# Optimization experiments

Hardware: AMD Instinct MI355X
Metric: run time of the kernel (lower is better)

## Reference

```python
import jax, jax.numpy as jnp
import numpy as np

N_NODES = 50000
N_EDGES = 800000


def _inv_sqrt_deg(idx, n):
    deg = jax.ops.segment_sum(jnp.ones(idx.shape, jnp.float32), idx, num_segments=n)
    return jnp.where(deg > 0, deg ** -0.5, 0.0)


def graph_conv(x, W, b, src, dst, norm_src, norm_dst):
    # DGL GraphConv, norm='both': D_dst^{-1/2} A D_src^{-1/2} X W + b
    # Apply weight before aggregation (out_feats < in_feats in both layers).
    h = (x * norm_src[:, None]) @ W            # [N, out]
    m = h[src]                                  # gather per-edge messages [E, out]
    agg = jax.ops.segment_sum(m, dst, num_segments=x.shape[0])
    return agg * norm_dst[:, None] + b


def setup_inputs() -> dict:
    key = jax.random.key(0)
    ks = jax.random.split(key, 6)
    x = jax.random.normal(ks[0], (N_NODES, 512), jnp.float32)
    W1 = jax.random.normal(ks[1], (512, 128), jnp.float32) * (512 ** -0.5)
    b1 = jnp.zeros((128,), jnp.float32)
    W2 = jax.random.normal(ks[2], (128, 40), jnp.float32) * (128 ** -0.5)
    b2 = jnp.zeros((40,), jnp.float32)
    src = jax.random.randint(ks[3], (N_EDGES,), 0, N_NODES, jnp.int32)
    dst = jax.random.randint(ks[4], (N_EDGES,), 0, N_NODES, jnp.int32)
    return {"x": x, "W1": W1, "b1": b1, "W2": W2, "b2": b2, "src": src, "dst": dst}


def reference(x, W1, b1, W2, b2, src, dst):
    n = x.shape[0]
    norm_src = _inv_sqrt_deg(src, n)  # out-degree based src norm
    norm_dst = _inv_sqrt_deg(dst, n)  # in-degree based dst norm
    h = graph_conv(x, W1, b1, src, dst, norm_src, norm_dst)
    h = jax.nn.relu(h)
    h = graph_conv(h, W2, b2, src, dst, norm_src, norm_dst)
    return h
```

## Files before the change

### kernel.cpp

```cpp
#include <hip/hip_runtime.h>
#include <hip/hip_bf16.h>

#define F0 512
#define F1 128
#define F2 40

#define NRP 12800
#define G_SL 64

typedef __attribute__((ext_vector_type(8))) short bf16x8;
typedef __attribute__((ext_vector_type(4))) float f32x4;

__device__ inline ushort f2bf(float f) {
    union { float f; uint u; } v; v.f = f;
    uint u = v.u;
    uint r = u + 0x7fffu + ((u >> 16) & 1u);
    return (ushort)(r >> 16);
}

#define CVT2(dst, a, b) { __hip_bfloat162 _t2 = __float22bfloat162_rn(make_float2(a, b)); __builtin_memcpy(&dst, &_t2, 4); }

__global__ __launch_bounds__(1024)
void hist_kernel(const int* __restrict__ src, const int* __restrict__ dst,
                 uchar* __restrict__ Gsrc, uchar* __restrict__ Gdst,
                 const float* __restrict__ W1, ushort* __restrict__ Wt, int n, int E) {
    if (blockIdx.x < (F0 * F1) / 1024) {
        int idx = blockIdx.x * 1024 + threadIdx.x;
        int k = idx >> 7, nn = idx & 127;
        Wt[nn * F0 + k] = f2bf(W1[idx]);
    }
    __shared__ uint cs[NRP / 2];
    __shared__ uint cd[NRP / 2];
    const int p = blockIdx.x / G_SL;
    const int g = blockIdx.x % G_SL;
    const int base = p * NRP;
    for (int i = threadIdx.x; i < NRP / 2; i += 1024) { cs[i] = 0; cd[i] = 0; }
    __syncthreads();
    const int Epg = (E + G_SL - 1) / G_SL;
    const int e0 = g * Epg;
    const int e1 = min(E, e0 + Epg);
    for (int i = e0 + (int)threadIdx.x; i < e1; i += 1024) {
        int s = src[i], d = dst[i];
        unsigned so = (unsigned)(s - base);
        unsigned dd = (unsigned)(d - base);
        if (so < (unsigned)NRP) atomicAdd(&cs[so >> 1], 1u << ((so & 1) * 16));
        if (dd < (unsigned)NRP) atomicAdd(&cd[dd >> 1], 1u << ((dd & 1) * 16));
    }
    __syncthreads();
    const int lim = min(NRP, n - base);
    for (int i = threadIdx.x; i < lim; i += 1024) {
        uint pcs = cs[i >> 1], pcd = cd[i >> 1];
        int sh = (i & 1) * 16;
        Gsrc[(size_t)g * n + base + i] = (uchar)((pcs >> sh) & 0xffu);
        Gdst[(size_t)g * n + base + i] = (uchar)((pcd >> sh) & 0xffu);
    }
}

__global__ __launch_bounds__(256)
void scanA_kernel(const uchar* __restrict__ Gsrc, const uchar* __restrict__ Gdst,
                  float* __restrict__ norm_src, float* __restrict__ norm_dst,
                  int* __restrict__ row_off, int* __restrict__ bsum, int n) {
    __shared__ int sm[256];
    int i = blockIdx.x * 256 + threadIdx.x;
    int s = 0, d = 0;
    if (i < n) {
#pragma unroll
        for (int g = 0; g < G_SL; g++) {
            s += Gsrc[(size_t)g * n + i];
            d += Gdst[(size_t)g * n + i];
        }
        norm_src[i] = s > 0 ? rsqrtf((float)s) : 0.f;
        norm_dst[i] = d > 0 ? rsqrtf((float)d) : 0.f;
    }
    sm[threadIdx.x] = (i < n) ? d : 0;
    __syncthreads();
    for (int off = 1; off < 256; off <<= 1) {
        int t = (threadIdx.x >= (unsigned)off) ? sm[threadIdx.x - off] : 0;
        __syncthreads();
        sm[threadIdx.x] += t;
        __syncthreads();
    }
    if (i < n) row_off[i + 1] = sm[threadIdx.x];
    if (threadIdx.x == 255) bsum[blockIdx.x] = sm[255];
}

__global__ __launch_bounds__(256)
void finalize_kernel(int* __restrict__ row_off, const int* __restrict__ bsum,
                     const uchar* __restrict__ Gdst, int* __restrict__ Goff, int n) {
    __shared__ int sm[256];
    const int b = blockIdx.x;
    const int t = threadIdx.x;
    sm[t] = (t < b) ? bsum[t] : 0;
    __syncthreads();
#pragma unroll
    for (int off = 128; off > 0; off >>= 1) {
        if (t < off) sm[t] += sm[t + off];
        __syncthreads();
    }
    const int excl = sm[0];
    const int v = b * 256 + t;
    if (v >= n) return;
    int raw = row_off[v];
    int start = excl + ((t == 0) ? 0 : raw);
    if (v == n - 1) {
        int rawn = row_off[n];
        row_off[n] = excl + rawn;
    }
    row_off[v] = start;
    int run = start;
#pragma unroll
    for (int g = 0; g < G_SL; g++) {
        size_t idx = (size_t)g * n + v;
        Goff[idx] = run;
        run += Gdst[idx];
    }
}

#define BM 64

union SmemU {
    int cur[NRP];
    char Al[2][8192];
};

#define ISSUE(kt, buf) {                                                               \
    __builtin_amdgcn_global_load_lds(                                                  \
        (const __attribute__((address_space(1))) void*)(gsrc_base + (kt) * 32),        \
        (__attribute__((address_space(3))) void*)(&smu.Al[buf][tid * 16]),             \
        16, 0, 0); }

#define LOADB(k0, b) { b = *reinterpret_cast<const bf16x8*>(bp + (k0)); }

#define MKFRAG(dst, mi, bufp) {                                                        \
    const int _row = (mi) * 16 + l15;                                                  \
    const char* _pr = (bufp) + _row * 128;                                             \
    float4 _pa = *reinterpret_cast<const float4*>(_pr + (((2 * lq + 0) ^ (_row & 7)) << 4)); \
    float4 _pb = *reinterpret_cast<const float4*>(_pr + (((2 * lq + 1) ^ (_row & 7)) << 4)); \
    union { uint u[4]; bf16x8 v; } _pk;                                                \
    CVT2(_pk.u[0], _pa.x, _pa.y); CVT2(_pk.u[1], _pa.z, _pa.w);                        \
    CVT2(_pk.u[2], _pb.x, _pb.y); CVT2(_pk.u[3], _pb.z, _pb.w);                        \
    dst = _pk.v; }

#define COMPUTE(buf, b) {                                                              \
    const char* _bp = &smu.Al[buf][0];                                                 \
    bf16x8 _a0, _a1, _a2, _a3;                                                         \
    MKFRAG(_a0, 0, _bp); MKFRAG(_a1, 1, _bp); MKFRAG(_a2, 2, _bp); MKFRAG(_a3, 3, _bp);\
    acc[0] = __builtin_amdgcn_mfma_f32_16x16x32_bf16(_a0, b, acc[0], 0, 0, 0);         \
    acc[1] = __builtin_amdgcn_mfma_f32_16x16x32_bf16(_a1, b, acc[1], 0, 0, 0);         \
    acc[2] = __builtin_amdgcn_mfma_f32_16x16x32_bf16(_a2, b, acc[2], 0, 0, 0);         \
    acc[3] = __builtin_amdgcn_mfma_f32_16x16x32_bf16(_a3, b, acc[3], 0, 0, 0); }

__global__ __launch_bounds__(512)
void place_gemm1_fused(const int* __restrict__ src, const int* __restrict__ dst,
                       const int* __restrict__ Goff, int* __restrict__ edge_src,
                       const float* __restrict__ x, const ushort* __restrict__ Wt,
                       const float* __restrict__ norm_src, ushort* __restrict__ h1g,
                       int n, int E, int ngemm) {
    __shared__ __align__(16) SmemU smu;
    const int tid = threadIdx.x;

    if (blockIdx.x >= ngemm) {
        const int pb = blockIdx.x - ngemm;
        const int p = pb / G_SL;
        const int g = pb % G_SL;
        const int base = p * NRP;
        const int lim = min(NRP, n - base);
        for (int i = tid; i < lim; i += 512)
            smu.cur[i] = Goff[(size_t)g * n + base + i];
        __syncthreads();
        const int Epg = (E + G_SL - 1) / G_SL;
        const int e0 = g * Epg;
        const int e1 = min(E, e0 + Epg);
        for (int i = e0 + tid; i < e1; i += 512) {
            int d = dst[i];
            unsigned dd = (unsigned)(d - base);
            if (dd < (unsigned)lim) {
                int pos = atomicAdd(&smu.cur[dd], 1);
                edge_src[pos] = src[i];
            }
        }
        return;
    }

    const int lane = tid & 63;
    const int w = tid >> 6;
    const int l15 = lane & 15;
    const int lq = lane >> 4;
    const int bm = blockIdx.x * BM;

    const int st_r = tid >> 3;
    const int st_c = (tid & 7) ^ (st_r & 7);
    int grow = bm + st_r;
    if (grow >= n) grow = n - 1;
    const float* gsrc_base = x + (size_t)grow * F0 + st_c * 4;

    const ushort* bp = Wt + (size_t)(w * 16 + l15) * F0 + lq * 8;

    f32x4 acc[4] = {};
    bf16x8 bcur, bnxt;

    ISSUE(0, 0);
    LOADB(0, bcur);
    __syncthreads();

    for (int kg = 0; kg < 16; ++kg) {
        const int cb = kg & 1;
        if (kg < 15) {
            ISSUE(kg + 1, cb ^ 1);
            LOADB((kg + 1) * 32, bnxt);
        }
        COMPUTE(cb, bcur);
        bcur = bnxt;
        if (kg < 15) __syncthreads();
    }

#pragma unroll
    for (int mi = 0; mi < 4; mi++) {
        int rbase = bm + mi * 16 + lq * 4;
#pragma unroll
        for (int r = 0; r < 4; r++) {
            int row = rbase + r;
            if (row < n) {
                float ns = norm_src[row];
                h1g[(size_t)row * F1 + w * 16 + l15] = f2bf(acc[mi][r] * ns);
            }
        }
    }
}

__global__ __launch_bounds__(256)
void agg1_kernel(const ushort* __restrict__ h1g, const int* __restrict__ row_off,
                 const int* __restrict__ edge_src, const float* __restrict__ norm_dst,
                 const float* __restrict__ b1, ushort* __restrict__ h1, int n) {
    int wid = (blockIdx.x * blockDim.x + threadIdx.x) >> 6;
    int lane = threadIdx.x & 63;
    if (wid >= n) return;
    int beg = row_off[wid], end = row_off[wid + 1];
    float a0 = 0.f, a1 = 0.f;
    int e = beg;
    for (; e + 7 < end; e += 8) {
        int s[8];
#pragma unroll
        for (int j = 0; j < 8; j++) s[j] = edge_src[e + j];
        uint v[8];
#pragma unroll
        for (int j = 0; j < 8; j++)
            v[j] = *reinterpret_cast<const uint*>(&h1g[(size_t)s[j] * F1 + lane * 2]);
#pragma unroll
        for (int j = 0; j < 8; j++) {
            a0 += __uint_as_float(v[j] << 16);
            a1 += __uint_as_float(v[j] & 0xffff0000u);
        }
    }
    for (; e < end; ++e) {
        int s = edge_src[e];
        uint v = *reinterpret_cast<const uint*>(&h1g[(size_t)s * F1 + lane * 2]);
        a0 += __uint_as_float(v << 16);
        a1 += __uint_as_float(v & 0xffff0000u);
    }
    float nd = norm_dst[wid];
    float o0 = fmaxf(a0 * nd + b1[lane * 2 + 0], 0.f);
    float o1 = fmaxf(a1 * nd + b1[lane * 2 + 1], 0.f);
    __hip_bfloat162 p2 = __float22bfloat162_rn(make_float2(o0, o1));
    uint pu; __builtin_memcpy(&pu, &p2, 4);
    *reinterpret_cast<uint*>(&h1[(size_t)wid * F1 + lane * 2]) = pu;
}

__global__ __launch_bounds__(256)
void gemm2_kernel(const ushort* __restrict__ h1, const float* __restrict__ W2,
                  const float* __restrict__ norm_src, ushort* __restrict__ h2g, int n) {
    __shared__ __align__(16) float W2s[F1][F2];
    for (int i = threadIdx.x; i < F1 * F2; i += 256)
        W2s[i / F2][i % F2] = W2[i];
    __syncthreads();
    int node = blockIdx.x * 256 + threadIdx.x;
    if (node >= n) return;
    float nrm = norm_src[node];
    f32x4 acc4[10] = {};
    const ushort* row = &h1[(size_t)node * F1];
    for (int kc = 0; kc < 16; kc++) {
        uint4 u = *reinterpret_cast<const uint4*>(&row[kc * 8]);
        uint uu[4] = {u.x, u.y, u.z, u.w};
        float f[8];
#pragma unroll
        for (int i = 0; i < 4; i++) {
            f[2 * i + 0] = __uint_as_float(uu[i] << 16);
            f[2 * i + 1] = __uint_as_float(uu[i] & 0xffff0000u);
        }
#pragma unroll
        for (int j = 0; j < 8; j++) {
#pragma unroll
            for (int c4 = 0; c4 < 10; c4++) {
                f32x4 wv = *reinterpret_cast<const f32x4*>(&W2s[kc * 8 + j][c4 * 4]);
                acc4[c4] += f[j] * wv;
            }
        }
    }
    ushort* orow = &h2g[(size_t)node * F2];
#pragma unroll
    for (int c4 = 0; c4 < 10; c4++) {
        f32x4 o = acc4[c4] * nrm;
        __hip_bfloat162 pa = __float22bfloat162_rn(make_float2(o[0], o[1]));
        __hip_bfloat162 pb = __float22bfloat162_rn(make_float2(o[2], o[3]));
        uint2 pk;
        __builtin_memcpy(&pk.x, &pa, 4);
        __builtin_memcpy(&pk.y, &pb, 4);
        *reinterpret_cast<uint2*>(&orow[c4 * 4]) = pk;
    }
}

__global__ __launch_bounds__(256)
void agg2_kernel(const ushort* __restrict__ h2g, const int* __restrict__ row_off,
                 const int* __restrict__ edge_src, const float* __restrict__ norm_dst,
                 const float* __restrict__ b2, float* __restrict__ out, int n) {
    int wid = (blockIdx.x * blockDim.x + threadIdx.x) >> 6;
    int lane = threadIdx.x & 63;
    if (wid >= n) return;
    int beg = row_off[wid], end = row_off[wid + 1];
    float a0 = 0.f, a1 = 0.f;
    int e = beg;
    const bool act = lane < 20;
    for (; e + 7 < end; e += 8) {
        int s[8];
#pragma unroll
        for (int j = 0; j < 8; j++) s[j] = edge_src[e + j];
        if (act) {
            uint v[8];
#pragma unroll
            for (int j = 0; j < 8; j++)
                v[j] = *reinterpret_cast<const uint*>(&h2g[(size_t)s[j] * F2 + lane * 2]);
#pragma unroll
            for (int j = 0; j < 8; j++) {
                a0 += __uint_as_float(v[j] << 16);
                a1 += __uint_as_float(v[j] & 0xffff0000u);
            }
        }
    }
    for (; e < end; ++e) {
        int s = edge_src[e];
        if (act) {
            uint v = *reinterpret_cast<const uint*>(&h2g[(size_t)s * F2 + lane * 2]);
            a0 += __uint_as_float(v << 16);
            a1 += __uint_as_float(v & 0xffff0000u);
        }
    }
    if (act) {
        float nd = norm_dst[wid];
        float o0 = a0 * nd + b2[lane * 2 + 0];
        float o1 = a1 * nd + b2[lane * 2 + 1];
        *reinterpret_cast<float2*>(&out[(size_t)wid * F2 + lane * 2]) = make_float2(o0, o1);
    }
}

extern "C" void kernel_launch(void* const* d_in, const int* in_sizes, int n_in,
                              void* d_out, int out_size, void* d_ws, size_t ws_size,
                              hipStream_t stream) {
    const float* x  = (const float*)d_in[0];
    const float* W1 = (const float*)d_in[1];
    const float* b1 = (const float*)d_in[2];
    const float* W2 = (const float*)d_in[3];
    const float* b2 = (const float*)d_in[4];
    const int* src  = (const int*)d_in[5];
    const int* dst  = (const int*)d_in[6];
    float* out = (float*)d_out;

    const int n = in_sizes[0] / F0;
    const int E = in_sizes[5];
    const int nb = (n + 255) / 256;
    const int P = (n + NRP - 1) / NRP;
    const int ngemm = (n + BM - 1) / BM;

    char* ws = (char*)d_ws;
    auto alloc = [&](size_t bytes) -> char* {
        char* p = ws;
        ws += (bytes + 255) & ~(size_t)255;
        return p;
    };
    int* row_off   = (int*)alloc((size_t)(n + 1) * 4);
    int* bsum      = (int*)alloc(256 * 4);
    int* edge_srcs = (int*)alloc((size_t)E * 4);
    float* norm_src_d = (float*)alloc((size_t)n * 4);
    float* norm_dst_d = (float*)alloc((size_t)n * 4);
    ushort* W1t = (ushort*)alloc((size_t)F1 * F0 * 2);
    ushort* h1g = (ushort*)alloc((size_t)n * F1 * 2);
    ushort* h1  = (ushort*)alloc((size_t)n * F1 * 2);
    ushort* h2g = h1g;

    uchar* Gsrc = (uchar*)h1g;
    uchar* Gdst = Gsrc + (size_t)G_SL * n;
    int* Goff = (int*)h1;

    hist_kernel<<<P * G_SL, 1024, 0, stream>>>(src, dst, Gsrc, Gdst, W1, W1t, n, E);
    scanA_kernel<<<nb, 256, 0, stream>>>(Gsrc, Gdst, norm_src_d, norm_dst_d, row_off, bsum, n);
    finalize_kernel<<<nb, 256, 0, stream>>>(row_off, bsum, Gdst, Goff, n);
    place_gemm1_fused<<<ngemm + P * G_SL, 512, 0, stream>>>(
        src, dst, Goff, edge_srcs, x, W1t, norm_src_d, h1g, n, E, ngemm);
    agg1_kernel<<<(n + 3) / 4, 256, 0, stream>>>(h1g, row_off, edge_srcs, norm_dst_d, b1, h1, n);
    gemm2_kernel<<<(n + 255) / 256, 256, 0, stream>>>(h1, W2, norm_src_d, h2g, n);
    agg2_kernel<<<(n + 3) / 4, 256, 0, stream>>>(h2g, row_off, edge_srcs, norm_dst_d, b2, out, n);
}
```

Before: 175.8 us.

## Deepen GEMM1 K-tile to 128 with four loads per stage, fewer barriers

Measured after the change: 181.7 us, median of 2. 3.3% more time.

```diff
diff --git a/kernel.cpp b/kernel.cpp
--- a/kernel.cpp
+++ b/kernel.cpp
@@ -117,38 +117,60 @@
 }
 
 #define BM 64
+#define NKT 4
 
 union SmemU {
     int cur[NRP];
-    char Al[2][8192];
+    char Al[2][32768];
 };
 
-#define ISSUE(kt, buf) {                                                               \
+#define ISSUE4(kt, buf) {                                                              \
     __builtin_amdgcn_global_load_lds(                                                  \
-        (const __attribute__((address_space(1))) void*)(gsrc_base + (kt) * 32),        \
+        (const __attribute__((address_space(1))) void*)(gs0 + (kt) * 128),             \
         (__attribute__((address_space(3))) void*)(&smu.Al[buf][tid * 16]),             \
+        16, 0, 0);                                                                     \
+    __builtin_amdgcn_global_load_lds(                                                  \
+        (const __attribute__((address_space(1))) void*)(gs1 + (kt) * 128),             \
+        (__attribute__((address_space(3))) void*)(&smu.Al[buf][8192 + tid * 16]),      \
+        16, 0, 0);                                                                     \
+    __builtin_amdgcn_global_load_lds(                                                  \
+        (const __attribute__((address_space(1))) void*)(gs2 + (kt) * 128),             \
+        (__attribute__((address_space(3))) void*)(&smu.Al[buf][16384 + tid * 16]),     \
+        16, 0, 0);                                                                     \
+    __builtin_amdgcn_global_load_lds(                                                  \
+        (const __attribute__((address_space(1))) void*)(gs3 + (kt) * 128),             \
+        (__attribute__((address_space(3))) void*)(&smu.Al[buf][24576 + tid * 16]),     \
         16, 0, 0); }
 
-#define LOADB(k0, b) { b = *reinterpret_cast<const bf16x8*>(bp + (k0)); }
-
-#define MKFRAG(dst, mi, bufp) {                                                        \
+#define LOADB4(kt, arr) {                                                              \
+    arr[0] = *reinterpret_cast<const bf16x8*>(bp + (kt) * 128 + 0);                    \
+    arr[1] = *reinterpret_cast<const bf16x8*>(bp + (kt) * 128 + 32);                   \
+    arr[2] = *reinterpret_cast<const bf16x8*>(bp + (kt) * 128 + 64);                   \
+    arr[3] = *reinterpret_cast<const bf16x8*>(bp + (kt) * 128 + 96); }
+
+#define MKFRAG(dst, mi, kk, bufp) {                                                    \
     const int _row = (mi) * 16 + l15;                                                  \
-    const char* _pr = (bufp) + _row * 128;                                             \
-    float4 _pa = *reinterpret_cast<const float4*>(_pr + (((2 * lq + 0) ^ (_row & 7)) << 4)); \
-    float4 _pb = *reinterpret_cast<const float4*>(_pr + (((2 * lq + 1) ^ (_row & 7)) << 4)); \
+    const char* _pr = (bufp) + _row * 512;                                             \
+    const int _sw = (l15 & 7) << 2;                                                    \
+    float4 _pa = *reinterpret_cast<const float4*>(_pr + ((((kk) * 8 + 2 * lq + 0) ^ _sw) << 4)); \
+    float4 _pb = *reinterpret_cast<const float4*>(_pr + ((((kk) * 8 + 2 * lq + 1) ^ _sw) << 4)); \
     union { uint u[4]; bf16x8 v; } _pk;                                                \
     CVT2(_pk.u[0], _pa.x, _pa.y); CVT2(_pk.u[1], _pa.z, _pa.w);                        \
     CVT2(_pk.u[2], _pb.x, _pb.y); CVT2(_pk.u[3], _pb.z, _pb.w);                        \
     dst = _pk.v; }
 
-#define COMPUTE(buf, b) {                                                              \
+#define COMPUTE16(buf, barr) {                                                         \
     const char* _bp = &smu.Al[buf][0];                                                 \
-    bf16x8 _a0, _a1, _a2, _a3;                                                         \
-    MKFRAG(_a0, 0, _bp); MKFRAG(_a1, 1, _bp); MKFRAG(_a2, 2, _bp); MKFRAG(_a3, 3, _bp);\
-    acc[0] = __builtin_amdgcn_mfma_f32_16x16x32_bf16(_a0, b, acc[0], 0, 0, 0);         \
-    acc[1] = __builtin_amdgcn_mfma_f32_16x16x32_bf16(_a1, b, acc[1], 0, 0, 0);         \
-    acc[2] = __builtin_amdgcn_mfma_f32_16x16x32_bf16(_a2, b, acc[2], 0, 0, 0);         \
-    acc[3] = __builtin_amdgcn_mfma_f32_16x16x32_bf16(_a3, b, acc[3], 0, 0, 0); }
+    _Pragma("unroll")                                                                  \
+    for (int kk = 0; kk < 4; ++kk) {                                                   \
+        bf16x8 _a0, _a1, _a2, _a3;                                                     \
+        MKFRAG(_a0, 0, kk, _bp); MKFRAG(_a1, 1, kk, _bp);                              \
+        MKFRAG(_a2, 2, kk, _bp); MKFRAG(_a3, 3, kk, _bp);                              \
+        acc[0] = __builtin_amdgcn_mfma_f32_16x16x32_bf16(_a0, barr[kk], acc[0], 0, 0, 0); \
+        acc[1] = __builtin_amdgcn_mfma_f32_16x16x32_bf16(_a1, barr[kk], acc[1], 0, 0, 0); \
+        acc[2] = __builtin_amdgcn_mfma_f32_16x16x32_bf16(_a2, barr[kk], acc[2], 0, 0, 0); \
+        acc[3] = __builtin_amdgcn_mfma_f32_16x16x32_bf16(_a3, barr[kk], acc[3], 0, 0, 0); \
+    } }
 
 __global__ __launch_bounds__(512)
 void place_gemm1_fused(const int* __restrict__ src, const int* __restrict__ dst,
@@ -188,30 +210,37 @@
     const int lq = lane >> 4;
     const int bm = blockIdx.x * BM;
 
-    const int st_r = tid >> 3;
-    const int st_c = (tid & 7) ^ (st_r & 7);
-    int grow = bm + st_r;
-    if (grow >= n) grow = n - 1;
-    const float* gsrc_base = x + (size_t)grow * F0 + st_c * 4;
+    const int st_sub = tid >> 5;
+    const int slot = tid & 31;
+    const int sslot = slot ^ ((st_sub & 7) << 2);
+    int g0 = bm + 0 * 16 + st_sub;  if (g0 >= n) g0 = n - 1;
+    int g1 = bm + 1 * 16 + st_sub;  if (g1 >= n) g1 = n - 1;
+    int g2 = bm + 2 * 16 + st_sub;  if (g2 >= n) g2 = n - 1;
+    int g3 = bm + 3 * 16 + st_sub;  if (g3 >= n) g3 = n - 1;
+    const float* gs0 = x + (size_t)g0 * F0 + sslot * 4;
+    const float* gs1 = x + (size_t)g1 * F0 + sslot * 4;
+    const float* gs2 = x + (size_t)g2 * F0 + sslot * 4;
+    const float* gs3 = x + (size_t)g3 * F0 + sslot * 4;
 
     const ushort* bp = Wt + (size_t)(w * 16 + l15) * F0 + lq * 8;
 
     f32x4 acc[4] = {};
-    bf16x8 bcur, bnxt;
-
-    ISSUE(0, 0);
-    LOADB(0, bcur);
-    __syncthreads();
-
-    for (int kg = 0; kg < 16; ++kg) {
-        const int cb = kg & 1;
-        if (kg < 15) {
-            ISSUE(kg + 1, cb ^ 1);
-            LOADB((kg + 1) * 32, bnxt);
-        }
-        COMPUTE(cb, bcur);
-        bcur = bnxt;
-        if (kg < 15) __syncthreads();
+    bf16x8 bcur[4], bnxt[4];
+
+    ISSUE4(0, 0);
+    LOADB4(0, bcur);
+    __syncthreads();
+
+    for (int kt = 0; kt < NKT; ++kt) {
+        const int cb = kt & 1;
+        if (kt < NKT - 1) {
+            ISSUE4(kt + 1, cb ^ 1);
+            LOADB4(kt + 1, bnxt);
+        }
+        COMPUTE16(cb, bcur);
+#pragma unroll
+        for (int j = 0; j < 4; ++j) bcur[j] = bnxt[j];
+        if (kt < NKT - 1) __syncthreads();
     }
 
 #pragma unroll
```

## Fuse layer-1 aggregation with layer-2 GEMM using MFMA on shared tile

Applied to the files above, without the earlier changes.

Measured after the change: 157.1 us. 1.12x faster.

```diff
diff --git a/kernel.cpp b/kernel.cpp
--- a/kernel.cpp
+++ b/kernel.cpp
@@ -23,11 +23,18 @@
 __global__ __launch_bounds__(1024)
 void hist_kernel(const int* __restrict__ src, const int* __restrict__ dst,
                  uchar* __restrict__ Gsrc, uchar* __restrict__ Gdst,
-                 const float* __restrict__ W1, ushort* __restrict__ Wt, int n, int E) {
+                 const float* __restrict__ W1, ushort* __restrict__ Wt,
+                 const float* __restrict__ W2, ushort* __restrict__ W2t, int n, int E) {
     if (blockIdx.x < (F0 * F1) / 1024) {
         int idx = blockIdx.x * 1024 + threadIdx.x;
         int k = idx >> 7, nn = idx & 127;
         Wt[nn * F0 + k] = f2bf(W1[idx]);
+    }
+    if (blockIdx.x == 64) {
+        for (int i = threadIdx.x; i < F1 * F2; i += 1024) {
+            int k = i / F2, c = i % F2;
+            W2t[c * F1 + k] = f2bf(W2[i]);
+        }
     }
     __shared__ uint cs[NRP / 2];
     __shared__ uint cd[NRP / 2];
@@ -229,83 +236,74 @@
 }
 
 __global__ __launch_bounds__(256)
-void agg1_kernel(const ushort* __restrict__ h1g, const int* __restrict__ row_off,
-                 const int* __restrict__ edge_src, const float* __restrict__ norm_dst,
-                 const float* __restrict__ b1, ushort* __restrict__ h1, int n) {
-    int wid = (blockIdx.x * blockDim.x + threadIdx.x) >> 6;
-    int lane = threadIdx.x & 63;
-    if (wid >= n) return;
-    int beg = row_off[wid], end = row_off[wid + 1];
-    float a0 = 0.f, a1 = 0.f;
-    int e = beg;
-    for (; e + 7 < end; e += 8) {
-        int s[8];
-#pragma unroll
-        for (int j = 0; j < 8; j++) s[j] = edge_src[e + j];
-        uint v[8];
-#pragma unroll
-        for (int j = 0; j < 8; j++)
-            v[j] = *reinterpret_cast<const uint*>(&h1g[(size_t)s[j] * F1 + lane * 2]);
-#pragma unroll
-        for (int j = 0; j < 8; j++) {
-            a0 += __uint_as_float(v[j] << 16);
-            a1 += __uint_as_float(v[j] & 0xffff0000u);
-        }
-    }
-    for (; e < end; ++e) {
-        int s = edge_src[e];
-        uint v = *reinterpret_cast<const uint*>(&h1g[(size_t)s * F1 + lane * 2]);
-        a0 += __uint_as_float(v << 16);
-        a1 += __uint_as_float(v & 0xffff0000u);
-    }
-    float nd = norm_dst[wid];
-    float o0 = fmaxf(a0 * nd + b1[lane * 2 + 0], 0.f);
-    float o1 = fmaxf(a1 * nd + b1[lane * 2 + 1], 0.f);
-    __hip_bfloat162 p2 = __float22bfloat162_rn(make_float2(o0, o1));
-    uint pu; __builtin_memcpy(&pu, &p2, 4);
-    *reinterpret_cast<uint*>(&h1[(size_t)wid * F1 + lane * 2]) = pu;
-}
-
-__global__ __launch_bounds__(256)
-void gemm2_kernel(const ushort* __restrict__ h1, const float* __restrict__ W2,
-                  const float* __restrict__ norm_src, ushort* __restrict__ h2g, int n) {
-    __shared__ __align__(16) float W2s[F1][F2];
-    for (int i = threadIdx.x; i < F1 * F2; i += 256)
-        W2s[i / F2][i % F2] = W2[i];
-    __syncthreads();
-    int node = blockIdx.x * 256 + threadIdx.x;
-    if (node >= n) return;
-    float nrm = norm_src[node];
-    f32x4 acc4[10] = {};
-    const ushort* row = &h1[(size_t)node * F1];
-    for (int kc = 0; kc < 16; kc++) {
-        uint4 u = *reinterpret_cast<const uint4*>(&row[kc * 8]);
-        uint uu[4] = {u.x, u.y, u.z, u.w};
-        float f[8];
-#pragma unroll
-        for (int i = 0; i < 4; i++) {
-            f[2 * i + 0] = __uint_as_float(uu[i] << 16);
-            f[2 * i + 1] = __uint_as_float(uu[i] & 0xffff0000u);
-        }
-#pragma unroll
-        for (int j = 0; j < 8; j++) {
-#pragma unroll
-            for (int c4 = 0; c4 < 10; c4++) {
-                f32x4 wv = *reinterpret_cast<const f32x4*>(&W2s[kc * 8 + j][c4 * 4]);
-                acc4[c4] += f[j] * wv;
-            }
-        }
-    }
-    ushort* orow = &h2g[(size_t)node * F2];
-#pragma unroll
-    for (int c4 = 0; c4 < 10; c4++) {
-        f32x4 o = acc4[c4] * nrm;
-        __hip_bfloat162 pa = __float22bfloat162_rn(make_float2(o[0], o[1]));
-        __hip_bfloat162 pb = __float22bfloat162_rn(make_float2(o[2], o[3]));
-        uint2 pk;
-        __builtin_memcpy(&pk.x, &pa, 4);
-        __builtin_memcpy(&pk.y, &pb, 4);
-        *reinterpret_cast<uint2*>(&orow[c4 * 4]) = pk;
+void agg1_gemm2_fused(const ushort* __restrict__ h1g, const int* __restrict__ row_off,
+                      const int* __restrict__ edge_src, const float* __restrict__ norm_dst,
+                      const float* __restrict__ b1, const ushort* __restrict__ W2t,
+                      const float* __restrict__ norm_src, ushort* __restrict__ h2g, int n) {
+    __shared__ __align__(16) char h1t[16 * 256];
+    const int tid = threadIdx.x;
+    const int lane = tid & 63;
+    const int w = tid >> 6;
+    const int l15 = lane & 15;
+    const int lq = lane >> 4;
+    const int nb0 = blockIdx.x * 16;
+
+    for (int i = 0; i < 4; ++i) {
+        const int r = w * 4 + i;
+        const int wid = nb0 + r;
+        float a0 = 0.f, a1 = 0.f;
+        if (wid < n) {
+            int beg = row_off[wid], end = row_off[wid + 1];
+            int e = beg;
+            for (; e + 7 < end; e += 8) {
+                int s[8];
+#pragma unroll
+                for (int j = 0; j < 8; j++) s[j] = edge_src[e + j];
+                uint v[8];
+#pragma unroll
+                for (int j = 0; j < 8; j++)
+                    v[j] = *reinterpret_cast<const uint*>(&h1g[(size_t)s[j] * F1 + lane * 2]);
+#pragma unroll
+                for (int j = 0; j < 8; j++) {
+                    a0 += __uint_as_float(v[j] << 16);
+                    a1 += __uint_as_float(v[j] & 0xffff0000u);
+                }
+            }
+            for (; e < end; ++e) {
+                int s = edge_src[e];
+                uint v = *reinterpret_cast<const uint*>(&h1g[(size_t)s * F1 + lane * 2]);
+                a0 += __uint_as_float(v << 16);
+                a1 += __uint_as_float(v & 0xffff0000u);
+            }
+            float nd = norm_dst[wid];
+            a0 = fmaxf(a0 * nd + b1[lane * 2 + 0], 0.f);
+            a1 = fmaxf(a1 * nd + b1[lane * 2 + 1], 0.f);
+        }
+        uint pu; CVT2(pu, a0, a1);
+        const int slotp = (lane >> 2) ^ (r & 7);
+        *reinterpret_cast<uint*>(h1t + r * 256 + slotp * 16 + (lane & 3) * 4) = pu;
+    }
+    __syncthreads();
+
+    if (w < 3) {
+        const int col = w * 16 + l15;
+        const int colc = (col < F2) ? col : (F2 - 1);
+        const ushort* bp = W2t + (size_t)colc * F1 + lq * 8;
+        f32x4 acc = {};
+#pragma unroll
+        for (int kk = 0; kk < 4; ++kk) {
+            const int slotp = (kk * 4 + lq) ^ (l15 & 7);
+            bf16x8 a = *reinterpret_cast<const bf16x8*>(h1t + l15 * 256 + slotp * 16);
+            bf16x8 b = *reinterpret_cast<const bf16x8*>(bp + kk * 32);
+            acc = __builtin_amdgcn_mfma_f32_16x16x32_bf16(a, b, acc, 0, 0, 0);
+        }
+#pragma unroll
+        for (int rr = 0; rr < 4; ++rr) {
+            int node = nb0 + lq * 4 + rr;
+            if (node < n && col < F2) {
+                h2g[(size_t)node * F2 + col] = f2bf(acc[rr] * norm_src[node]);
+            }
+        }
     }
 }
 
@@ -382,20 +380,21 @@
     float* norm_src_d = (float*)alloc((size_t)n * 4);
     float* norm_dst_d = (float*)alloc((size_t)n * 4);
     ushort* W1t = (ushort*)alloc((size_t)F1 * F0 * 2);
+    ushort* W2t = (ushort*)alloc((size_t)F2 * F1 * 2);
     ushort* h1g = (ushort*)alloc((size_t)n * F1 * 2);
-    ushort* h1  = (ushort*)alloc((size_t)n * F1 * 2);
-    ushort* h2g = h1g;
+    char*  scratch = alloc((size_t)G_SL * n * 4);
 
     uchar* Gsrc = (uchar*)h1g;
     uchar* Gdst = Gsrc + (size_t)G_SL * n;
-    int* Goff = (int*)h1;
-
-    hist_kernel<<<P * G_SL, 1024, 0, stream>>>(src, dst, Gsrc, Gdst, W1, W1t, n, E);
+    int* Goff = (int*)scratch;
+    ushort* h2g = (ushort*)scratch;
+
+    hist_kernel<<<P * G_SL, 1024, 0, stream>>>(src, dst, Gsrc, Gdst, W1, W1t, W2, W2t, n, E);
     scanA_kernel<<<nb, 256, 0, stream>>>(Gsrc, Gdst, norm_src_d, norm_dst_d, row_off, bsum, n);
     finalize_kernel<<<nb, 256, 0, stream>>>(row_off, bsum, Gdst, Goff, n);
     place_gemm1_fused<<<ngemm + P * G_SL, 512, 0, stream>>>(
         src, dst, Goff, edge_srcs, x, W1t, norm_src_d, h1g, n, E, ngemm);
-    agg1_kernel<<<(n + 3) / 4, 256, 0, stream>>>(h1g, row_off, edge_srcs, norm_dst_d, b1, h1, n);
-    gemm2_kernel<<<(n + 255) / 256, 256, 0, stream>>>(h1, W2, norm_src_d, h2g, n);
+    agg1_gemm2_fused<<<(n + 15) / 16, 256, 0, stream>>>(
+        h1g, row_off, edge_srcs, norm_dst_d, b1, W2t, norm_src_d, h2g, n);
     agg2_kernel<<<(n + 3) / 4, 256, 0, stream>>>(h2g, row_off, edge_srcs, norm_dst_d, b2, out, n);
 }
```
